# Optimization experiments

Measured on AMD Instinct MI355X. Metric: run time of the kernel, lower is better.

The kernel has to match this reference:

```python
import jax, jax.numpy as jnp
import numpy as np

PRIMES = (1, 2654435761, 805459861, 3674653429)
N_PTS = 400000


def _flat_index(c, res, T, tiled):
    # c: [N, D] uint32 integer grid coords; returns int32 table indices in [0, T).
    Tm = jnp.uint32(T - 1)  # T is a power of two
    prod = int(np.prod(np.asarray(res, dtype=np.int64)))
    if tiled or prod <= T:
        strides = np.cumprod([1] + list(res[:-1])).astype(np.uint32)
        idx = jnp.sum(c * jnp.asarray(strides), axis=1)
    else:
        ps = jnp.asarray(np.array(PRIMES[: c.shape[1]], dtype=np.uint32))
        terms = c * ps
        idx = terms[:, 0]
        for d in range(1, c.shape[1]):
            idx = idx ^ terms[:, d]
    return (idx & Tm).astype(jnp.int32)


def grid_encode(x, table, base, growth, tiled=False, nearest=False):
    # x: [N, D] in [0,1); table: [L, T, F] -> [N, L*F]
    N, D = x.shape
    L, T, F = table.shape
    outs = []
    for l in range(L):
        res = [int(np.ceil(b * g ** l)) for b, g in zip(base, growth)]
        res_f = jnp.asarray(np.array(res, np.float32))
        pos = x * (res_f - 1.0)  # [N, D]
        if nearest:
            c = jnp.clip(jnp.rint(pos), 0.0, res_f - 1.0).astype(jnp.uint32)
            feat = table[l][_flat_index(c, res, T, tiled)]
        else:
            p0 = jnp.floor(pos)
            w = pos - p0  # trilinear weights, [N, D]
            feat = jnp.zeros((N, F), table.dtype)
            for corner in range(1 << D):
                offs = np.array([(corner >> d) & 1 for d in range(D)], np.float32)
                c = jnp.minimum(p0 + offs, res_f - 1.0).astype(jnp.uint32)
                wt = jnp.prod(jnp.where(offs > 0, w, 1.0 - w), axis=1, keepdims=True)
                feat = feat + wt * table[l][_flat_index(c, res, T, tiled)]
        outs.append(feat)
    return jnp.concatenate(outs, axis=1)


def setup_inputs() -> dict:
    key = jax.random.key(0)
    kx, ks, kt, km = jax.random.split(key, 4)
    x = jax.random.uniform(kx, (N_PTS, 4), dtype=jnp.float32)
    table_s = jax.random.normal(ks, (16, 1 << 19, 2), dtype=jnp.float32) * 0.1
    table_t = jax.random.normal(kt, (16, 1 << 19, 2), dtype=jnp.float32) * 0.1
    table_m = jax.random.normal(km, (1, 1 << 21, 1), dtype=jnp.float32) * 0.1
    return {"x": x, "table_s": table_s, "table_t": table_t, "table_m": table_m}


def reference(x, table_s, table_t, table_m):
    s_base, s_g = (16, 16, 16), (1.2, 1.2, 1.2)
    t_base, t_g = (16, 16, 16, 16), (1.2, 1.2, 1.2, 1.2)
    m_base, m_g = (128, 128, 128), (1.0, 1.0, 1.0)
    s = grid_encode(x[:, :3], table_s, s_base, s_g)                       # [N, 32]
    t = grid_encode(x, table_t, t_base, t_g)                              # [N, 32]
    m = jax.nn.sigmoid(grid_encode(x[:, :3], table_m, m_base, m_g, tiled=True, nearest=True))  # [N, 1]
    return s + t * (1.0 - m)
```

## Files before the change

kernel.cpp:

```cpp
#include <hip/hip_runtime.h>
#include <cstdint>

#define NLEV 16
#define TMASK ((1u << 19) - 1u)

typedef float f4v __attribute__((ext_vector_type(4)));
typedef float f2v __attribute__((ext_vector_type(2)));
typedef uint32_t u2v __attribute__((ext_vector_type(2)));

__constant__ int c_res[NLEV] = {16, 20, 24, 28, 34, 40, 48, 58, 69, 83,
                                100, 119, 143, 172, 206, 247};

__device__ __forceinline__ float bf_lo(uint32_t e) { return __uint_as_float(e << 16); }
__device__ __forceinline__ float bf_hi(uint32_t e) { return __uint_as_float(e & 0xFFFF0000u); }
__device__ __forceinline__ uint32_t rne16(float f) {
    uint32_t u = __float_as_uint(f);
    return (u + 0x7fffu + ((u >> 16) & 1u)) >> 16;
}

__global__ __launch_bounds__(256) void conv_kernel(
    const f4v* __restrict__ src_s, const f4v* __restrict__ src_t,
    u2v* __restrict__ dst_s, u2v* __restrict__ dst_t, int half)
{
    int i = blockIdx.x * 256 + threadIdx.x;
    const f4v* src = (i < half) ? src_s : src_t;
    u2v* dst = (i < half) ? dst_s : dst_t;
    int j = (i < half) ? i : i - half;
    if (j < half) {
        f4v v = __builtin_nontemporal_load(src + j);
        u2v o;
        o.x = rne16(v.x) | (rne16(v.y) << 16);
        o.y = rne16(v.z) | (rne16(v.w) << 16);
        __builtin_nontemporal_store(o, dst + j);
    }
}

__global__ __launch_bounds__(256) void m_kernel(
    const float* __restrict__ x, const float* __restrict__ tab_m,
    float* __restrict__ one_m, int N)
{
    int n = blockIdx.x * 256 + threadIdx.x;
    if (n >= N) return;
    f4v xv = __builtin_nontemporal_load((const f4v*)x + n);
    float q0 = fminf(fmaxf(rintf(xv.x * 127.0f), 0.0f), 127.0f);
    float q1 = fminf(fmaxf(rintf(xv.y * 127.0f), 0.0f), 127.0f);
    float q2 = fminf(fmaxf(rintf(xv.z * 127.0f), 0.0f), 127.0f);
    uint32_t idx = (uint32_t)q0 + ((uint32_t)q1 << 7) + ((uint32_t)q2 << 14);
    float v = tab_m[idx];
    float m = 1.0f / (1.0f + expf(-v));
    __builtin_nontemporal_store(1.0f - m, one_m + n);
}

template<bool IS_T>
__global__ __launch_bounds__(256, 4) void enc_kernel(
    const float* __restrict__ x,
    const uint32_t* __restrict__ tab,
    const float* __restrict__ one_m,
    f2v* __restrict__ ws, int N, int half_grid)
{
    const int NP = IS_T ? 8 : 4;

    int blk = blockIdx.x;
    int hi = (blk >= half_grid) ? 1 : 0;
    int blkp = blk - hi * half_grid;
    int l = (blkp & 7) + hi * 8;
    int n = ((blkp >> 3) << 8) + threadIdx.x;
    if (n >= N) return;

    f4v xv = __builtin_nontemporal_load((const f4v*)x + n);

    int r = c_res[l];
    uint32_t ru = (uint32_t)r;
    float rf1 = (float)r - 1.0f;

    float p0 = xv.x * rf1, p1 = xv.y * rf1, p2 = xv.z * rf1;
    float f0 = floorf(p0), f1 = floorf(p1), f2 = floorf(p2);
    float w0 = p0 - f0, w1 = p1 - f1, w2 = p2 - f2;
    uint32_t c0a = (uint32_t)f0;

    float p3 = 0.0f, f3 = 0.0f, w3 = 0.0f;
    if (IS_T) { p3 = xv.w * rf1; f3 = floorf(p3); w3 = p3 - f3; }

    const bool direct = IS_T ? (l <= 2) : (l <= 8);
    const uint32_t* tl = tab + ((size_t)l << 19);

    uint32_t idxa[8];
    uint32_t oidx[8];
    uint32_t need[8];
    #pragma unroll
    for (int pi = 0; pi < NP; ++pi) {
        float o1 = (float)(pi & 1);
        float o2 = (float)((pi >> 1) & 1);
        uint32_t c1 = (uint32_t)fminf(f1 + o1, rf1);
        uint32_t c2 = (uint32_t)fminf(f2 + o2, rf1);
        if (direct) {
            uint32_t base;
            if (IS_T) {
                float o3 = (float)((pi >> 2) & 1);
                uint32_t c3 = (uint32_t)fminf(f3 + o3, rf1);
                base = ru * (c1 + ru * (c2 + ru * c3));
            } else {
                base = ru * (c1 + ru * c2);
            }
            uint32_t ia = base + c0a;
            idxa[pi] = ia;
            oidx[pi] = ia + 1;
            need[pi] = ia & 1;
        } else {
            uint32_t hh = (c1 * 2654435761u) ^ (c2 * 805459861u);
            if (IS_T) {
                float o3 = (float)((pi >> 2) & 1);
                uint32_t c3 = (uint32_t)fminf(f3 + o3, rf1);
                hh ^= c3 * 3674653429u;
            }
            idxa[pi] = (c0a ^ hh) & TMASK;
            oidx[pi] = ((c0a + 1) ^ hh) & TMASK;
            need[pi] = c0a & 1;
        }
    }

    u2v pv[8];
    #pragma unroll
    for (int pi = 0; pi < NP; ++pi)
        pv[pi] = *(const u2v*)(tl + (idxa[pi] & ~1u));
    uint32_t ov[8];
    #pragma unroll
    for (int pi = 0; pi < NP; ++pi)
        if (need[pi]) ov[pi] = tl[oidx[pi]];

    float a0 = 0.0f, a1 = 0.0f;
    float wva = 1.0f - w0, wvb = w0;
    #pragma unroll
    for (int pi = 0; pi < NP; ++pi) {
        float bw = ((pi & 1) ? w1 : 1.0f - w1)
                 * (((pi >> 1) & 1) ? w2 : 1.0f - w2);
        if (IS_T) bw *= (((pi >> 2) & 1) ? w3 : 1.0f - w3);
        uint32_t sw = idxa[pi] & 1;
        uint32_t ea = sw ? pv[pi].y : pv[pi].x;
        uint32_t eb = sw ? pv[pi].x : pv[pi].y;
        if (need[pi]) eb = ov[pi];
        float wa = bw * wva, wb = bw * wvb;
        a0 += wa * bf_lo(ea) + wb * bf_lo(eb);
        a1 += wa * bf_hi(ea) + wb * bf_hi(eb);
    }

    if (IS_T) {
        float om = __builtin_nontemporal_load(one_m + n);
        f2v outv; outv.x = a0 * om; outv.y = a1 * om;
        __builtin_nontemporal_store(outv, ws + (size_t)l * N + n);
    } else {
        size_t i = (size_t)l * N + n;
        f2v prev = __builtin_nontemporal_load(ws + i);
        f2v outv; outv.x = prev.x + a0; outv.y = prev.y + a1;
        __builtin_nontemporal_store(outv, ws + i);
    }
}

__global__ __launch_bounds__(256) void out_kernel(
    const f2v* __restrict__ ws, f4v* __restrict__ out4, int N)
{
    __shared__ float lds[256 * 33];
    int tid = threadIdx.x;
    int n = (blockIdx.x << 8) + tid;

    if (n < N) {
        #pragma unroll
        for (int l = 0; l < NLEV; ++l) {
            f2v v = __builtin_nontemporal_load(ws + (size_t)l * N + n);
            lds[tid * 33 + 2 * l]     = v.x;
            lds[tid * 33 + 2 * l + 1] = v.y;
        }
    }
    __syncthreads();

    size_t out4base = (size_t)blockIdx.x * 2048;
    size_t limit = (size_t)N * 8;
    #pragma unroll
    for (int k = 0; k < 8; ++k) {
        int g = k * 256 + tid;
        size_t G = out4base + g;
        if (G < limit) {
            int p = g >> 3;
            int e = (g & 7) * 4;
            f4v v;
            v.x = lds[p * 33 + e];
            v.y = lds[p * 33 + e + 1];
            v.z = lds[p * 33 + e + 2];
            v.w = lds[p * 33 + e + 3];
            __builtin_nontemporal_store(v, out4 + G);
        }
    }
}

__global__ __launch_bounds__(256) void grid_enc_kernel(
    const float* __restrict__ x,
    const float* __restrict__ tab_s,
    const float* __restrict__ tab_t,
    const float* __restrict__ tab_m,
    float* __restrict__ out, int N)
{
    int tid = blockIdx.x * blockDim.x + threadIdx.x;
    if (tid >= N * NLEV) return;
    int n = tid >> 4, l = tid & 15;
    float x0 = x[n*4+0], x1 = x[n*4+1], x2 = x[n*4+2], x3 = x[n*4+3];
    float one_m;
    {
        float q0 = fminf(fmaxf(rintf(x0*127.0f),0.0f),127.0f);
        float q1 = fminf(fmaxf(rintf(x1*127.0f),0.0f),127.0f);
        float q2 = fminf(fmaxf(rintf(x2*127.0f),0.0f),127.0f);
        uint32_t idx = (uint32_t)q0 + ((uint32_t)q1<<7) + ((uint32_t)q2<<14);
        one_m = 1.0f - 1.0f/(1.0f + expf(-tab_m[idx]));
    }
    int r = c_res[l]; uint32_t ru = (uint32_t)r; float rf1 = (float)r - 1.0f;
    float p0 = x0*rf1, p1 = x1*rf1, p2 = x2*rf1, p3 = x3*rf1;
    float f0 = floorf(p0), f1 = floorf(p1), f2 = floorf(p2), f3 = floorf(p3);
    float w0 = p0-f0, w1 = p1-f1, w2 = p2-f2, w3 = p3-f3;
    const float2* ts2 = (const float2*)tab_s + ((size_t)l<<19);
    const float2* tt2 = (const float2*)tab_t + ((size_t)l<<19);
    const bool sd = (l<=8), td = (l<=2);
    float s0=0,s1=0;
    #pragma unroll
    for (int c = 0; c < 8; ++c) {
        uint32_t c0 = (uint32_t)fminf(f0+(float)(c&1), rf1);
        uint32_t c1 = (uint32_t)fminf(f1+(float)((c>>1)&1), rf1);
        uint32_t c2 = (uint32_t)fminf(f2+(float)((c>>2)&1), rf1);
        float wt = ((c&1)?w0:1.0f-w0)*(((c>>1)&1)?w1:1.0f-w1)*(((c>>2)&1)?w2:1.0f-w2);
        uint32_t idx = sd ? (c0 + c1*ru + c2*ru*ru)
                          : (c0 ^ (c1*2654435761u) ^ (c2*805459861u));
        float2 e = ts2[idx & TMASK]; s0 += wt*e.x; s1 += wt*e.y;
    }
    float t0=0,t1=0;
    #pragma unroll
    for (int c = 0; c < 16; ++c) {
        uint32_t c0 = (uint32_t)fminf(f0+(float)(c&1), rf1);
        uint32_t c1 = (uint32_t)fminf(f1+(float)((c>>1)&1), rf1);
        uint32_t c2 = (uint32_t)fminf(f2+(float)((c>>2)&1), rf1);
        uint32_t c3 = (uint32_t)fminf(f3+(float)((c>>3)&1), rf1);
        float wt = ((c&1)?w0:1.0f-w0)*(((c>>1)&1)?w1:1.0f-w1)
                 *(((c>>2)&1)?w2:1.0f-w2)*(((c>>3)&1)?w3:1.0f-w3);
        uint32_t idx = td ? (c0 + ru*(c1 + ru*(c2 + ru*c3)))
                          : (c0 ^ (c1*2654435761u) ^ (c2*805459861u) ^ (c3*3674653429u));
        float2 e = tt2[idx & TMASK]; t0 += wt*e.x; t1 += wt*e.y;
    }
    size_t o = (size_t)n*32 + 2*(size_t)l;
    out[o] = s0 + t0*one_m; out[o+1] = s1 + t1*one_m;
}

extern "C" void kernel_launch(void* const* d_in, const int* in_sizes, int n_in,
                              void* d_out, int out_size, void* d_ws, size_t ws_size,
                              hipStream_t stream) {
    const float* x     = (const float*)d_in[0];
    const float* tab_s = (const float*)d_in[1];
    const float* tab_t = (const float*)d_in[2];
    const float* tab_m = (const float*)d_in[3];
    float* out = (float*)d_out;

    int N = in_sizes[0] / 4;
    size_t wm_b = (((size_t)N * 4) + 255) & ~(size_t)255;
    size_t wc_b = (size_t)N * NLEV * 8;
    size_t tb_b = (size_t)NLEV * (1u << 19) * 4;
    int nchunk = (N + 255) / 256;

    if (ws_size >= wm_b + wc_b + 2 * tb_b) {
        float* wm = (float*)d_ws;
        f2v*   wc = (f2v*)((char*)d_ws + wm_b);
        uint32_t* ps = (uint32_t*)((char*)d_ws + wm_b + wc_b);
        uint32_t* pt = ps + (size_t)NLEV * (1u << 19);
        int half = NLEV * (1 << 19) / 2;
        int half_grid = 8 * nchunk;
        conv_kernel<<<(2 * half + 255) / 256, 256, 0, stream>>>(
            (const f4v*)tab_s, (const f4v*)tab_t, (u2v*)ps, (u2v*)pt, half);
        m_kernel<<<nchunk, 256, 0, stream>>>(x, tab_m, wm, N);
        enc_kernel<true><<<16 * nchunk, 256, 0, stream>>>(x, pt, wm, wc, N, half_grid);
        enc_kernel<false><<<16 * nchunk, 256, 0, stream>>>(x, ps, wm, wc, N, half_grid);
        out_kernel<<<nchunk, 256, 0, stream>>>(wc, (f4v*)out, N);
    } else {
        int total = N * NLEV;
        grid_enc_kernel<<<(total + 255) / 256, 256, 0, stream>>>(x, tab_s, tab_t, tab_m, out, N);
    }
}
```

Measured before the change: 685.0 us.

## Fuse spatial and temporal encode kernels into a single per-level kernel

Merges the two per-table encode kernels into one that computes both the 3D spatial and 4D temporal trilinear lookups for each point and level. The spatial result is combined with the temporal result times (1-m) in registers. This removes one launch, one full write of the workspace and its read-modify-write pass, and the second load of x. It raises per-thread register use (12 corner loads in flight) while increasing launch_bounds min-blocks from 4 to 6, so spilling or register pressure is a risk.

```diff
diff --git a/kernel.cpp b/kernel.cpp
--- a/kernel.cpp
+++ b/kernel.cpp
@@ -51,15 +51,13 @@
     __builtin_nontemporal_store(1.0f - m, one_m + n);
 }
 
-template<bool IS_T>
-__global__ __launch_bounds__(256, 4) void enc_kernel(
+__global__ __launch_bounds__(256, 6) void enc_fused(
     const float* __restrict__ x,
-    const uint32_t* __restrict__ tab,
+    const uint32_t* __restrict__ tabS,
+    const uint32_t* __restrict__ tabT,
     const float* __restrict__ one_m,
     f2v* __restrict__ ws, int N, int half_grid)
 {
-    const int NP = IS_T ? 8 : 4;
-
     int blk = blockIdx.x;
     int hi = (blk >= half_grid) ? 1 : 0;
     int blkp = blk - hi * half_grid;
@@ -67,93 +65,112 @@
     int n = ((blkp >> 3) << 8) + threadIdx.x;
     if (n >= N) return;
 
-    f4v xv = __builtin_nontemporal_load((const f4v*)x + n);
-
     int r = c_res[l];
     uint32_t ru = (uint32_t)r;
     float rf1 = (float)r - 1.0f;
-
-    float p0 = xv.x * rf1, p1 = xv.y * rf1, p2 = xv.z * rf1;
-    float f0 = floorf(p0), f1 = floorf(p1), f2 = floorf(p2);
-    float w0 = p0 - f0, w1 = p1 - f1, w2 = p2 - f2;
+    const bool dirS = (l <= 8), dirT = (l <= 2);
+    const uint32_t* tlS = tabS + ((size_t)l << 19);
+    const uint32_t* tlT = tabT + ((size_t)l << 19);
+
+    f4v xv = __builtin_nontemporal_load((const f4v*)x + n);
+
+    float p0 = xv.x * rf1, p1 = xv.y * rf1, p2 = xv.z * rf1, p3 = xv.w * rf1;
+    float f0 = floorf(p0), f1 = floorf(p1), f2 = floorf(p2), f3 = floorf(p3);
+    float w0 = p0 - f0, w1 = p1 - f1, w2 = p2 - f2, w3 = p3 - f3;
     uint32_t c0a = (uint32_t)f0;
 
-    float p3 = 0.0f, f3 = 0.0f, w3 = 0.0f;
-    if (IS_T) { p3 = xv.w * rf1; f3 = floorf(p3); w3 = p3 - f3; }
-
-    const bool direct = IS_T ? (l <= 2) : (l <= 8);
-    const uint32_t* tl = tab + ((size_t)l << 19);
-
-    uint32_t idxa[8];
-    uint32_t oidx[8];
-    uint32_t need[8];
-    #pragma unroll
-    for (int pi = 0; pi < NP; ++pi) {
+    u2v pvT[8];
+    uint32_t ovT[8];
+    uint32_t swT = 0u, nbT = 0u;
+    #pragma unroll
+    for (int pi = 0; pi < 8; ++pi) {
+        float o1 = (float)(pi & 1);
+        float o2 = (float)((pi >> 1) & 1);
+        float o3 = (float)((pi >> 2) & 1);
+        uint32_t c1 = (uint32_t)fminf(f1 + o1, rf1);
+        uint32_t c2 = (uint32_t)fminf(f2 + o2, rf1);
+        uint32_t c3 = (uint32_t)fminf(f3 + o3, rf1);
+        uint32_t ia, ib, needi;
+        if (dirT) {
+            uint32_t base = ru * (c1 + ru * (c2 + ru * c3));
+            ia = base + c0a;
+            ib = ia + 1;
+            needi = ia & 1u;
+        } else {
+            uint32_t hh = (c1 * 2654435761u) ^ (c2 * 805459861u)
+                        ^ (c3 * 3674653429u);
+            ia = (c0a ^ hh) & TMASK;
+            ib = ((c0a + 1u) ^ hh) & TMASK;
+            needi = c0a & 1u;
+        }
+        pvT[pi] = *(const u2v*)(tlT + (ia & ~1u));
+        if (needi) ovT[pi] = tlT[ib];
+        swT |= (ia & 1u) << pi;
+        nbT |= needi << pi;
+    }
+
+    u2v pvS[4];
+    uint32_t ovS[4];
+    uint32_t swS = 0u, nbS = 0u;
+    #pragma unroll
+    for (int pi = 0; pi < 4; ++pi) {
         float o1 = (float)(pi & 1);
         float o2 = (float)((pi >> 1) & 1);
         uint32_t c1 = (uint32_t)fminf(f1 + o1, rf1);
         uint32_t c2 = (uint32_t)fminf(f2 + o2, rf1);
-        if (direct) {
-            uint32_t base;
-            if (IS_T) {
-                float o3 = (float)((pi >> 2) & 1);
-                uint32_t c3 = (uint32_t)fminf(f3 + o3, rf1);
-                base = ru * (c1 + ru * (c2 + ru * c3));
-            } else {
-                base = ru * (c1 + ru * c2);
-            }
-            uint32_t ia = base + c0a;
-            idxa[pi] = ia;
-            oidx[pi] = ia + 1;
-            need[pi] = ia & 1;
+        uint32_t ia, ib, needi;
+        if (dirS) {
+            uint32_t base = ru * (c1 + ru * c2);
+            ia = base + c0a;
+            ib = ia + 1;
+            needi = ia & 1u;
         } else {
             uint32_t hh = (c1 * 2654435761u) ^ (c2 * 805459861u);
-            if (IS_T) {
-                float o3 = (float)((pi >> 2) & 1);
-                uint32_t c3 = (uint32_t)fminf(f3 + o3, rf1);
-                hh ^= c3 * 3674653429u;
-            }
-            idxa[pi] = (c0a ^ hh) & TMASK;
-            oidx[pi] = ((c0a + 1) ^ hh) & TMASK;
-            need[pi] = c0a & 1;
-        }
-    }
-
-    u2v pv[8];
-    #pragma unroll
-    for (int pi = 0; pi < NP; ++pi)
-        pv[pi] = *(const u2v*)(tl + (idxa[pi] & ~1u));
-    uint32_t ov[8];
-    #pragma unroll
-    for (int pi = 0; pi < NP; ++pi)
-        if (need[pi]) ov[pi] = tl[oidx[pi]];
-
-    float a0 = 0.0f, a1 = 0.0f;
+            ia = (c0a ^ hh) & TMASK;
+            ib = ((c0a + 1u) ^ hh) & TMASK;
+            needi = c0a & 1u;
+        }
+        pvS[pi] = *(const u2v*)(tlS + (ia & ~1u));
+        if (needi) ovS[pi] = tlS[ib];
+        swS |= (ia & 1u) << pi;
+        nbS |= needi << pi;
+    }
+
+    float om = __builtin_nontemporal_load(one_m + n);
+
+    float t0 = 0.0f, t1 = 0.0f;
     float wva = 1.0f - w0, wvb = w0;
     #pragma unroll
-    for (int pi = 0; pi < NP; ++pi) {
+    for (int pi = 0; pi < 8; ++pi) {
+        float bw = ((pi & 1) ? w1 : 1.0f - w1)
+                 * (((pi >> 1) & 1) ? w2 : 1.0f - w2)
+                 * (((pi >> 2) & 1) ? w3 : 1.0f - w3);
+        uint32_t sw = (swT >> pi) & 1u;
+        uint32_t ea = sw ? pvT[pi].y : pvT[pi].x;
+        uint32_t eb = sw ? pvT[pi].x : pvT[pi].y;
+        if ((nbT >> pi) & 1u) eb = ovT[pi];
+        float wa = bw * wva, wb = bw * wvb;
+        t0 += wa * bf_lo(ea) + wb * bf_lo(eb);
+        t1 += wa * bf_hi(ea) + wb * bf_hi(eb);
+    }
+    float s0 = 0.0f, s1 = 0.0f;
+    #pragma unroll
+    for (int pi = 0; pi < 4; ++pi) {
         float bw = ((pi & 1) ? w1 : 1.0f - w1)
                  * (((pi >> 1) & 1) ? w2 : 1.0f - w2);
-        if (IS_T) bw *= (((pi >> 2) & 1) ? w3 : 1.0f - w3);
-        uint32_t sw = idxa[pi] & 1;
-        uint32_t ea = sw ? pv[pi].y : pv[pi].x;
-        uint32_t eb = sw ? pv[pi].x : pv[pi].y;
-        if (need[pi]) eb = ov[pi];
+        uint32_t sw = (swS >> pi) & 1u;
+        uint32_t ea = sw ? pvS[pi].y : pvS[pi].x;
+        uint32_t eb = sw ? pvS[pi].x : pvS[pi].y;
+        if ((nbS >> pi) & 1u) eb = ovS[pi];
         float wa = bw * wva, wb = bw * wvb;
-        a0 += wa * bf_lo(ea) + wb * bf_lo(eb);
-        a1 += wa * bf_hi(ea) + wb * bf_hi(eb);
-    }
-
-    if (IS_T) {
-        float om = __builtin_nontemporal_load(one_m + n);
-        f2v outv; outv.x = a0 * om; outv.y = a1 * om;
-        __builtin_nontemporal_store(outv, ws + (size_t)l * N + n);
-    } else {
-        size_t i = (size_t)l * N + n;
-        f2v prev = __builtin_nontemporal_load(ws + i);
-        f2v outv; outv.x = prev.x + a0; outv.y = prev.y + a1;
-        __builtin_nontemporal_store(outv, ws + i);
-    }
+        s0 += wa * bf_lo(ea) + wb * bf_lo(eb);
+        s1 += wa * bf_hi(ea) + wb * bf_hi(eb);
+    }
+
+    f2v outv;
+    outv.x = s0 + t0 * om;
+    outv.y = s1 + t1 * om;
+    __builtin_nontemporal_store(outv, ws + (size_t)l * N + n);
 }
 
 __global__ __launch_bounds__(256) void out_kernel(
@@ -271,8 +288,7 @@
         conv_kernel<<<(2 * half + 255) / 256, 256, 0, stream>>>(
             (const f4v*)tab_s, (const f4v*)tab_t, (u2v*)ps, (u2v*)pt, half);
         m_kernel<<<nchunk, 256, 0, stream>>>(x, tab_m, wm, N);
-        enc_kernel<true><<<16 * nchunk, 256, 0, stream>>>(x, pt, wm, wc, N, half_grid);
-        enc_kernel<false><<<16 * nchunk, 256, 0, stream>>>(x, ps, wm, wc, N, half_grid);
+        enc_fused<<<16 * nchunk, 256, 0, stream>>>(x, ps, pt, wm, wc, N, half_grid);
         out_kernel<<<nchunk, 256, 0, stream>>>(wc, (f4v*)out, N);
     } else {
         int total = N * NLEV;
```

After: 603.9 us. -11.8%, faster.
